# Kernel optimization log

Measured on AMD Instinct MI355X. Metric: run time of the kernel, lower is better.

## Reference

```python
import jax, jax.numpy as jnp
import numpy as np

H = 256           # hidden_size
D_IN = 4 * H      # 1024
D_K = 8 * H       # 2048
B, N = 8, 2048


def setup_inputs() -> dict:
    key = jax.random.key(0)
    ks = jax.random.split(key, 7)
    s_in = 1.0 / np.sqrt(D_IN)
    s_dk = 1.0 / np.sqrt(D_K)
    x = jax.random.normal(ks[0], (B, N, D_IN), dtype=jnp.float32)
    Wq = jax.random.uniform(ks[1], (D_IN, D_K), jnp.float32, -s_in, s_in)
    Wk = jax.random.uniform(ks[2], (D_IN, D_K), jnp.float32, -s_in, s_in)
    Wv = jax.random.uniform(ks[3], (D_IN, D_K), jnp.float32, -s_in, s_in)
    Wfc = jax.random.uniform(ks[4], (D_K, D_IN), jnp.float32, -s_dk, s_dk)
    bfc = jax.random.uniform(ks[5], (D_IN,), jnp.float32, -s_dk, s_dk)
    gamma = jnp.ones((D_IN,), jnp.float32)
    beta = jnp.zeros((D_IN,), jnp.float32)
    return {"x": x, "Wq": Wq, "Wk": Wk, "Wv": Wv, "Wfc": Wfc,
            "bfc": bfc, "gamma": gamma, "beta": beta}


def layer_norm(y, gamma, beta, eps=1e-5):
    mu = jnp.mean(y, axis=-1, keepdims=True)
    var = jnp.var(y, axis=-1, keepdims=True)
    return (y - mu) * jax.lax.rsqrt(var + eps) * gamma + beta


def reference(x, Wq, Wk, Wv, Wfc, bfc, gamma, beta):
    # Q/K/V projections: [B, N, D_K]
    q = jnp.einsum('bnd,dk->bnk', x, Wq)
    k = jnp.einsum('bnd,dk->bnk', x, Wk)
    v = jnp.einsum('bnd,dk->bnk', x, Wv)
    # NOTE: original module has NO 1/sqrt(d_k) scaling — keep it faithful.
    scores = jnp.einsum('bnk,bmk->bnm', q, k)           # [B, N, N]
    attn = jax.nn.softmax(scores, axis=-1)
    att_x = jnp.einsum('bnm,bmk->bnk', attn, v)          # [B, N, D_K]
    h = jax.nn.relu(jnp.einsum('bnk,kd->bnd', att_x, Wfc) + bfc)
    return layer_norm(x + h, gamma, beta)
```

## Files before the change

kernel.cpp:

```cpp
#include <hip/hip_runtime.h>
#include <stdint.h>


#define DEVI __device__ __forceinline__

typedef uint16_t u16;
typedef _Float16 f16x8 __attribute__((ext_vector_type(8)));
typedef float f32x4 __attribute__((ext_vector_type(4)));

DEVI u16 f2h(float f) {
  union { _Float16 h; u16 u; } v;
  v.h = (_Float16)f;
  return v.u;
}
DEVI float h2f(u16 x) {
  union { _Float16 h; u16 u; } v;
  v.u = x;
  return (float)v.h;
}

DEVI void gload_lds16(const void* g, void* lds) {
  __builtin_amdgcn_global_load_lds(
      (const __attribute__((address_space(1))) void*)g,
      (__attribute__((address_space(3))) void*)lds, 16, 0, 0);
}

template <int EPI>
__global__ __launch_bounds__(512, 2) void gemm8p(
    const u16* __restrict__ A, const u16* __restrict__ B, void* __restrict__ C,
    int K, int lda, int ldb, int ldc,
    long aZ, long bZ, long cZ,
    const float* __restrict__ bias, const float* __restrict__ xres)
{
  __shared__ u16 lds[2 * 32768];
  char* ldsB = (char*)lds;
  const int tid = threadIdx.x;
  const int bz = blockIdx.z;

  const int gx = gridDim.x;
  int fl = blockIdx.y * gx + blockIdx.x;
  const int cpx = (gx * gridDim.y) >> 3;
  fl = (fl & 7) * cpx + (fl >> 3);
  const int bx = fl % gx, by = fl / gx;

  const u16* Ab = A + (long)bz * aZ + (long)(by * 256) * lda;
  const u16* Bb = B + (long)bz * bZ + (long)(bx * 256) * ldb;

  const int wid = tid >> 6, lane = tid & 63;
  const int wm = wid >> 2, wn = wid & 3;
  const int l15 = lane & 15;

  int aBase[2][2]; long aoff[2][2];
  int bBase[2][2]; long boff[2][2];
#pragma unroll
  for (int h = 0; h < 2; ++h) {
#pragma unroll
    for (int j = 0; j < 2; ++j) {
      const int s = wid * 2 + j;
      int rs = (s < 8) ? (64 * h + s * 8) : (128 + 64 * h + (s - 8) * 8);
      aBase[h][j] = rs * 128;
      {
        const int d = rs * 128 + lane * 16;
        const int dl = d ^ (((d >> 7) & 7) << 4);
        aoff[h][j] = (long)(dl >> 7) * (lda * 2) + (dl & 127);
      }
      rs = 64 * (s >> 2) + 32 * h + (s & 3) * 8;
      bBase[h][j] = 32768 + rs * 128;
      {
        const int d = rs * 128 + lane * 16;
        const int dl = d ^ (((d >> 7) & 7) << 4);
        boff[h][j] = (long)(dl >> 7) * (ldb * 2) + (dl & 127);
      }
    }
  }

  const int swz = (lane & 7) << 4;
  const int ko0 = ((lane >> 4) * 16) ^ swz;
  const int ko1 = (64 + (lane >> 4) * 16) ^ swz;

  f32x4 acc[8][4] = {};

  auto STAGE_A = [&](int t, int h) {
    char* dst = ldsB + (t & 1) * 65536;
    const long kB = (long)t * 128;
#pragma unroll
    for (int j = 0; j < 2; ++j)
      gload_lds16((const char*)Ab + aoff[h][j] + kB, dst + aBase[h][j]);
  };
  auto STAGE_B = [&](int t, int h) {
    char* dst = ldsB + (t & 1) * 65536;
    const long kB = (long)t * 128;
#pragma unroll
    for (int j = 0; j < 2; ++j)
      gload_lds16((const char*)Bb + boff[h][j] + kB, dst + bBase[h][j]);
  };

  const int NT = K >> 6;
  STAGE_A(0, 0); STAGE_B(0, 0); STAGE_B(0, 1); STAGE_A(0, 1);

  for (int t = 0; t < NT; ++t) {
    const bool more = (t + 1 < NT);
    const char* ab = ldsB + (t & 1) * 65536;
    const char* bb = ab + 32768;
    f16x8 af[8], bf0[4], bf1[4];

    asm volatile("s_waitcnt vmcnt(4)" ::: "memory");
    __builtin_amdgcn_s_barrier();
    if (more) STAGE_A(t + 1, 0);
#pragma unroll
    for (int m = 0; m < 4; ++m) {
      const char* r = ab + (wm * 128 + m * 16 + l15) * 128;
      af[2 * m] = *(const f16x8*)(r + ko0);
      af[2 * m + 1] = *(const f16x8*)(r + ko1);
    }
#pragma unroll
    for (int n = 0; n < 2; ++n) {
      const char* r = bb + (wn * 64 + n * 16 + l15) * 128;
      bf0[2 * n] = *(const f16x8*)(r + ko0);
      bf0[2 * n + 1] = *(const f16x8*)(r + ko1);
    }
    __builtin_amdgcn_s_setprio(1);
#pragma unroll
    for (int ks = 0; ks < 2; ++ks)
#pragma unroll
      for (int m = 0; m < 4; ++m)
#pragma unroll
        for (int n = 0; n < 2; ++n)
          acc[m][n] = __builtin_amdgcn_mfma_f32_16x16x32_f16(
              af[2 * m + ks], bf0[2 * n + ks], acc[m][n], 0, 0, 0);
    __builtin_amdgcn_s_setprio(0);

    if (more) asm volatile("s_waitcnt vmcnt(4)" ::: "memory");
    else      asm volatile("s_waitcnt vmcnt(2)" ::: "memory");
    __builtin_amdgcn_s_barrier();
    if (more) STAGE_B(t + 1, 0);
#pragma unroll
    for (int n = 0; n < 2; ++n) {
      const char* r = bb + (wn * 64 + (n + 2) * 16 + l15) * 128;
      bf1[2 * n] = *(const f16x8*)(r + ko0);
      bf1[2 * n + 1] = *(const f16x8*)(r + ko1);
    }
    __builtin_amdgcn_s_setprio(1);
#pragma unroll
    for (int ks = 0; ks < 2; ++ks)
#pragma unroll
      for (int m = 0; m < 4; ++m)
#pragma unroll
        for (int n = 0; n < 2; ++n)
          acc[m][n + 2] = __builtin_amdgcn_mfma_f32_16x16x32_f16(
              af[2 * m + ks], bf1[2 * n + ks], acc[m][n + 2], 0, 0, 0);
    __builtin_amdgcn_s_setprio(0);

    if (more) asm volatile("s_waitcnt vmcnt(4)" ::: "memory");
    else      asm volatile("s_waitcnt vmcnt(0)" ::: "memory");
    __builtin_amdgcn_s_barrier();
    if (more) STAGE_B(t + 1, 1);
#pragma unroll
    for (int m = 0; m < 4; ++m) {
      const char* r = ab + (wm * 128 + (m + 4) * 16 + l15) * 128;
      af[2 * m] = *(const f16x8*)(r + ko0);
      af[2 * m + 1] = *(const f16x8*)(r + ko1);
    }
    __builtin_amdgcn_s_setprio(1);
#pragma unroll
    for (int ks = 0; ks < 2; ++ks)
#pragma unroll
      for (int m = 0; m < 4; ++m)
#pragma unroll
        for (int n = 0; n < 2; ++n)
          acc[m + 4][n] = __builtin_amdgcn_mfma_f32_16x16x32_f16(
              af[2 * m + ks], bf0[2 * n + ks], acc[m + 4][n], 0, 0, 0);
    __builtin_amdgcn_s_setprio(0);
    if (more) STAGE_A(t + 1, 1);
    __builtin_amdgcn_s_setprio(1);
#pragma unroll
    for (int ks = 0; ks < 2; ++ks)
#pragma unroll
      for (int m = 0; m < 4; ++m)
#pragma unroll
        for (int n = 0; n < 2; ++n)
          acc[m + 4][n + 2] = __builtin_amdgcn_mfma_f32_16x16x32_f16(
              af[2 * m + ks], bf1[2 * n + ks], acc[m + 4][n + 2], 0, 0, 0);
    __builtin_amdgcn_s_setprio(0);
  }

  const long cBase = (long)bz * cZ;
  const int rowBase = by * 256 + wm * 128;
  const int colBase = bx * 256 + wn * 64;

  if constexpr (EPI == 3) {
    u16* vT = (u16*)C;
#pragma unroll
    for (int m = 0; m < 8; ++m) {
      const long row0 = rowBase + m * 16 + (lane >> 4) * 4;
      const long bb2 = (row0 >> 11) * 4194304L + (row0 & 2047);
#pragma unroll
      for (int n = 0; n < 4; ++n) {
        const int col = colBase + n * 16 + l15;
        ushort4 h;
        h.x = f2h(acc[m][n][0]); h.y = f2h(acc[m][n][1]);
        h.z = f2h(acc[m][n][2]); h.w = f2h(acc[m][n][3]);
        *(ushort4*)(vT + bb2 + (long)col * 2048) = h;
      }
    }
  } else {
#pragma unroll
    for (int m = 0; m < 8; ++m) {
#pragma unroll
      for (int r = 0; r < 4; ++r) {
        const long row = rowBase + m * 16 + (lane >> 4) * 4 + r;
#pragma unroll
        for (int n = 0; n < 4; ++n) {
          const int col = colBase + n * 16 + l15;
          float v = acc[m][n][r];
          if constexpr (EPI == 0) {
            ((u16*)C)[cBase + row * ldc + col] = f2h(v);
          } else {
            v += bias[col];
            v = fmaxf(v, 0.0f);
            v += xres[row * (long)ldc + col];
            ((float*)C)[row * (long)ldc + col] = v;
          }
        }
      }
    }
  }
}

template <int EPI>
__global__ __launch_bounds__(256) void gemm_bt(
    const u16* __restrict__ A, const u16* __restrict__ B, void* __restrict__ C,
    int K, int lda, int ldb, int ldc,
    long aZ, long bZ, long cZ,
    const float* __restrict__ bias, const float* __restrict__ xres)
{
  __shared__ u16 sA[128 * 32];
  __shared__ u16 sB[128 * 32];
  const int tid = threadIdx.x;
  const int bz = blockIdx.z;
  const u16* Ab = A + (long)bz * aZ + (long)(blockIdx.y * 128) * lda;
  const u16* Bb = B + (long)bz * bZ + (long)(blockIdx.x * 128) * ldb;

  const int lane = tid & 63;
  const int wr = (tid >> 7) & 1;
  const int wc = (tid >> 6) & 1;
  const int l15 = lane & 15, l4 = lane >> 4;

  const int f0 = tid, f1 = tid + 256;
  const long ga0 = (long)(f0 >> 2) * lda + (f0 & 3) * 8;
  const long ga1 = (long)(f1 >> 2) * lda + (f1 & 3) * 8;
  const long gb0 = (long)(f0 >> 2) * ldb + (f0 & 3) * 8;
  const long gb1 = (long)(f1 >> 2) * ldb + (f1 & 3) * 8;
  u16* sAd0 = sA + (tid & ~63) * 8;
  u16* sAd1 = sA + 2048 + (tid & ~63) * 8;
  u16* sBd0 = sB + (tid & ~63) * 8;
  u16* sBd1 = sB + 2048 + (tid & ~63) * 8;

  f32x4 acc[4][4] = {};

  for (int k0 = 0; k0 < K; k0 += 32) {
    gload_lds16(Ab + ga0 + k0, sAd0);
    gload_lds16(Ab + ga1 + k0, sAd1);
    gload_lds16(Bb + gb0 + k0, sBd0);
    gload_lds16(Bb + gb1 + k0, sBd1);
    __syncthreads();
    f16x8 af[4], bf[4];
#pragma unroll
    for (int m = 0; m < 4; ++m)
      af[m] = *(const f16x8*)(sA + (wr * 64 + m * 16 + l15) * 32 + l4 * 8);
#pragma unroll
    for (int n = 0; n < 4; ++n)
      bf[n] = *(const f16x8*)(sB + (wc * 64 + n * 16 + l15) * 32 + l4 * 8);
#pragma unroll
    for (int m = 0; m < 4; ++m)
#pragma unroll
      for (int n = 0; n < 4; ++n)
        acc[m][n] = __builtin_amdgcn_mfma_f32_16x16x32_f16(af[m], bf[n], acc[m][n], 0, 0, 0);
    __syncthreads();
  }

  const long cBase = (long)bz * cZ;
  const int rowBase = blockIdx.y * 128 + wr * 64;
  const int colBase = blockIdx.x * 128 + wc * 64;

#pragma unroll
  for (int m = 0; m < 4; ++m) {
#pragma unroll
    for (int r = 0; r < 4; ++r) {
      const long row = rowBase + m * 16 + l4 * 4 + r;
#pragma unroll
      for (int n = 0; n < 4; ++n) {
        const int col = colBase + n * 16 + l15;
        float v = acc[m][n][r];
        if constexpr (EPI == 0) {
          ((u16*)C)[cBase + row * ldc + col] = f2h(v);
        } else if constexpr (EPI == 1) {
          ((float*)C)[cBase + row * ldc + col] = v;
        } else {
          v += bias[col];
          v = fmaxf(v, 0.0f);
          v += xres[row * (long)ldc + col];
          ((float*)C)[row * (long)ldc + col] = v;
        }
      }
    }
  }
}

__global__ __launch_bounds__(256) void softmax_rows16(u16* __restrict__ sc)
{
  const long row = blockIdx.x;
  u16* p = sc + row * 2048;
  const int tid = threadIdx.x;
  uint4 w = ((const uint4*)p)[tid];
  float e[8];
  e[0] = h2f(w.x & 0xffff); e[1] = h2f(w.x >> 16);
  e[2] = h2f(w.y & 0xffff); e[3] = h2f(w.y >> 16);
  e[4] = h2f(w.z & 0xffff); e[5] = h2f(w.z >> 16);
  e[6] = h2f(w.w & 0xffff); e[7] = h2f(w.w >> 16);
  float m = fmaxf(fmaxf(fmaxf(e[0], e[1]), fmaxf(e[2], e[3])),
                  fmaxf(fmaxf(e[4], e[5]), fmaxf(e[6], e[7])));
#pragma unroll
  for (int o = 32; o; o >>= 1) m = fmaxf(m, __shfl_xor(m, o));
  __shared__ float redm[4];
  if ((tid & 63) == 0) redm[tid >> 6] = m;
  __syncthreads();
  m = fmaxf(fmaxf(redm[0], redm[1]), fmaxf(redm[2], redm[3]));

  float s = 0.0f;
#pragma unroll
  for (int i = 0; i < 8; ++i) { e[i] = __expf(e[i] - m); s += e[i]; }
#pragma unroll
  for (int o = 32; o; o >>= 1) s += __shfl_xor(s, o);
  __shared__ float reds[4];
  if ((tid & 63) == 0) reds[tid >> 6] = s;
  __syncthreads();
  s = (reds[0] + reds[1]) + (reds[2] + reds[3]);
  const float inv = 1.0f / s;

  uint4 o;
  o.x = (uint32_t)f2h(e[0] * inv) | ((uint32_t)f2h(e[1] * inv) << 16);
  o.y = (uint32_t)f2h(e[2] * inv) | ((uint32_t)f2h(e[3] * inv) << 16);
  o.z = (uint32_t)f2h(e[4] * inv) | ((uint32_t)f2h(e[5] * inv) << 16);
  o.w = (uint32_t)f2h(e[6] * inv) | ((uint32_t)f2h(e[7] * inv) << 16);
  ((uint4*)p)[tid] = o;
}

__global__ __launch_bounds__(256) void softmax_rows(float* __restrict__ scores)
{
  const long row = blockIdx.x;
  const float* src = scores + row * 2048;
  const int tid = threadIdx.x;
  float4 a = ((const float4*)src)[tid];
  float4 b = ((const float4*)src)[tid + 256];
  float m = fmaxf(fmaxf(fmaxf(a.x, a.y), fmaxf(a.z, a.w)),
                  fmaxf(fmaxf(b.x, b.y), fmaxf(b.z, b.w)));
#pragma unroll
  for (int o = 32; o; o >>= 1) m = fmaxf(m, __shfl_xor(m, o));
  __shared__ float redm[4];
  if ((tid & 63) == 0) redm[tid >> 6] = m;
  __syncthreads();
  m = fmaxf(fmaxf(redm[0], redm[1]), fmaxf(redm[2], redm[3]));

  float e[8];
  e[0] = __expf(a.x - m); e[1] = __expf(a.y - m);
  e[2] = __expf(a.z - m); e[3] = __expf(a.w - m);
  e[4] = __expf(b.x - m); e[5] = __expf(b.y - m);
  e[6] = __expf(b.z - m); e[7] = __expf(b.w - m);
  float s = ((e[0] + e[1]) + (e[2] + e[3])) + ((e[4] + e[5]) + (e[6] + e[7]));
#pragma unroll
  for (int o = 32; o; o >>= 1) s += __shfl_xor(s, o);
  __shared__ float reds[4];
  if ((tid & 63) == 0) reds[tid >> 6] = s;
  __syncthreads();
  s = (reds[0] + reds[1]) + (reds[2] + reds[3]);
  const float inv = 1.0f / s;

  u16* dst = (u16*)scores + row * 4096;
  uint2 w0, w1;
  w0.x = (uint32_t)f2h(e[0] * inv) | ((uint32_t)f2h(e[1] * inv) << 16);
  w0.y = (uint32_t)f2h(e[2] * inv) | ((uint32_t)f2h(e[3] * inv) << 16);
  w1.x = (uint32_t)f2h(e[4] * inv) | ((uint32_t)f2h(e[5] * inv) << 16);
  w1.y = (uint32_t)f2h(e[6] * inv) | ((uint32_t)f2h(e[7] * inv) << 16);
  ((uint2*)dst)[tid] = w0;
  ((uint2*)dst)[tid + 256] = w1;
}

__global__ __launch_bounds__(256) void layernorm_rows(
    const float* __restrict__ y, const float* __restrict__ gamma,
    const float* __restrict__ beta, float* __restrict__ out)
{
  const long row = blockIdx.x;
  const int tid = threadIdx.x;
  float4 v = ((const float4*)(y + row * 1024))[tid];
  float s = (v.x + v.y) + (v.z + v.w);
  float q = (v.x * v.x + v.y * v.y) + (v.z * v.z + v.w * v.w);
#pragma unroll
  for (int o = 32; o; o >>= 1) { s += __shfl_xor(s, o); q += __shfl_xor(q, o); }
  __shared__ float rs[4], rq[4];
  if ((tid & 63) == 0) { rs[tid >> 6] = s; rq[tid >> 6] = q; }
  __syncthreads();
  s = (rs[0] + rs[1]) + (rs[2] + rs[3]);
  q = (rq[0] + rq[1]) + (rq[2] + rq[3]);
  const float mu = s * (1.0f / 1024.0f);
  const float var = q * (1.0f / 1024.0f) - mu * mu;
  const float rstd = rsqrtf(var + 1e-5f);
  float4 g = ((const float4*)gamma)[tid];
  float4 be = ((const float4*)beta)[tid];
  float4 o;
  o.x = (v.x - mu) * rstd * g.x + be.x;
  o.y = (v.y - mu) * rstd * g.y + be.y;
  o.z = (v.z - mu) * rstd * g.z + be.z;
  o.w = (v.w - mu) * rstd * g.w + be.w;
  __syncthreads();
  ((float4*)(out + row * 1024))[tid] = o;
}

__global__ __launch_bounds__(256) void cvt_f32_f16(
    const float* __restrict__ in, u16* __restrict__ out, long n4)
{
  const long stride = (long)gridDim.x * 256;
  for (long i = (long)blockIdx.x * 256 + threadIdx.x; i < n4; i += stride) {
    float4 v = ((const float4*)in)[i];
    uint2 p;
    p.x = (uint32_t)f2h(v.x) | ((uint32_t)f2h(v.y) << 16);
    p.y = (uint32_t)f2h(v.z) | ((uint32_t)f2h(v.w) << 16);
    ((uint2*)out)[i] = p;
  }
}

__global__ __launch_bounds__(256) void tw_f32(
    const float* __restrict__ in, u16* __restrict__ out, int R, int C)
{
  __shared__ float T[32][33];
  const int c0 = blockIdx.x * 32, r0 = blockIdx.y * 32;
  const int tx = threadIdx.x & 31, ty = threadIdx.x >> 5;
#pragma unroll
  for (int i = 0; i < 4; ++i)
    T[ty + i * 8][tx] = in[(long)(r0 + ty + i * 8) * C + c0 + tx];
  __syncthreads();
#pragma unroll
  for (int i = 0; i < 4; ++i)
    out[(long)(c0 + ty + i * 8) * R + r0 + tx] = f2h(T[tx][ty + i * 8]);
}

__global__ __launch_bounds__(256) void transpose_u16(
    const u16* __restrict__ in, u16* __restrict__ out, int R, int C)
{
  __shared__ u16 T[32][33];
  const long zo = (long)blockIdx.z * R * C;
  const int c0 = blockIdx.x * 32, r0 = blockIdx.y * 32;
  const int tx = threadIdx.x & 31, ty = threadIdx.x >> 5;
#pragma unroll
  for (int i = 0; i < 4; ++i)
    T[ty + i * 8][tx] = in[zo + (long)(r0 + ty + i * 8) * C + c0 + tx];
  __syncthreads();
#pragma unroll
  for (int i = 0; i < 4; ++i)
    out[zo + (long)(c0 + ty + i * 8) * R + r0 + tx] = T[tx][ty + i * 8];
}

extern "C" void kernel_launch(void* const* d_in, const int* in_sizes, int n_in,
                              void* d_out, int out_size, void* d_ws, size_t ws_size,
                              hipStream_t stream)
{
  const float* x     = (const float*)d_in[0];
  const float* Wq    = (const float*)d_in[1];
  const float* Wk    = (const float*)d_in[2];
  const float* Wv    = (const float*)d_in[3];
  const float* Wfc   = (const float*)d_in[4];
  const float* bfc   = (const float*)d_in[5];
  const float* gamma = (const float*)d_in[6];
  const float* beta  = (const float*)d_in[7];
  float* out = (float*)d_out;

  char* ws = (char*)d_ws;

  u16* wqkvT = (u16*)(ws + 0);
  u16* wfcT  = (u16*)(ws + 12582912);
  tw_f32<<<dim3(64, 32), 256, 0, stream>>>(Wq, wqkvT, 1024, 2048);
  tw_f32<<<dim3(64, 32), 256, 0, stream>>>(Wk, wqkvT + (long)2048 * 1024, 1024, 2048);
  tw_f32<<<dim3(64, 32), 256, 0, stream>>>(Wv, wqkvT + (long)2 * 2048 * 1024, 1024, 2048);
  tw_f32<<<dim3(32, 64), 256, 0, stream>>>(Wfc, wfcT, 2048, 1024);

  if (ws_size >= 251658240ULL) {
    u16*  q_   = (u16*)(ws + 16777216);
    u16*  k_   = (u16*)(ws + 83886080);
    u16*  vT   = (u16*)(ws + 150994944);
    u16*  sc16 = (u16*)(ws + 218103808);
    u16*  xb   = sc16;

    cvt_f32_f16<<<2048, 256, 0, stream>>>(x, xb, (long)16384 * 1024 / 4);

    gemm8p<0><<<dim3(8, 64, 2), 512, 0, stream>>>(
        xb, wqkvT, (void*)q_, 1024, 1024, 1024, 2048,
        0L, (long)2048 * 1024, (long)16384 * 2048, nullptr, nullptr);
    gemm8p<3><<<dim3(8, 64, 1), 512, 0, stream>>>(
        xb, wqkvT + (long)2 * 2048 * 1024, (void*)vT, 1024, 1024, 1024, 2048,
        0L, 0L, 0L, nullptr, nullptr);

    for (int c = 0; c < 2; ++c) {
      const u16* qc = q_ + (long)c * 1024 * 2048;
      gemm8p<0><<<dim3(8, 4, 8), 512, 0, stream>>>(
          qc, k_, (void*)sc16, 2048, 2048, 2048, 2048,
          (long)2048 * 2048, (long)2048 * 2048, (long)1024 * 2048, nullptr, nullptr);
      softmax_rows16<<<8192, 256, 0, stream>>>(sc16);
      gemm8p<0><<<dim3(8, 4, 8), 512, 0, stream>>>(
          sc16, vT, (void*)(q_ + (long)c * 1024 * 2048), 2048, 2048, 2048, 2048,
          (long)1024 * 2048, (long)2048 * 2048, (long)2048 * 2048, nullptr, nullptr);
    }

    gemm8p<2><<<dim3(4, 64, 1), 512, 0, stream>>>(
        q_, wfcT, (void*)out, 2048, 2048, 2048, 1024,
        0L, 0L, 0L, bfc, x);
  } else if (ws_size >= 109051904ULL) {
    u16*  xb2 = (u16*)(ws + 16777216);
    u16*  q2  = (u16*)(ws + 25165824);
    u16*  k2  = q2 + (long)2 * 2048 * 2048;
    u16*  v2  = q2 + (long)4 * 2048 * 2048;
    float* sc2 = (float*)(ws + 75497472);
    u16*  vT2   = k2;
    u16*  attx2 = q2;

    for (int p = 0; p < 4; ++p) {
      const float* xp = x + (long)p * 4096 * 1024;
      cvt_f32_f16<<<1024, 256, 0, stream>>>(xp, xb2, (long)4096 * 1024 / 4);
      for (int b = 0; b < 2; ++b)
        gemm_bt<0><<<dim3(16, 16, 3), 256, 0, stream>>>(
            xb2 + (long)b * 2048 * 1024, wqkvT, (void*)(q2 + (long)b * 2048 * 2048),
            1024, 1024, 1024, 2048,
            0L, (long)2048 * 1024, (long)2 * 2048 * 2048, nullptr, nullptr);
      gemm_bt<1><<<dim3(16, 16, 2), 256, 0, stream>>>(
          q2, k2, (void*)sc2, 2048, 2048, 2048, 2048,
          (long)2048 * 2048, (long)2048 * 2048, (long)2048 * 2048, nullptr, nullptr);
      softmax_rows<<<4096, 256, 0, stream>>>(sc2);
      transpose_u16<<<dim3(64, 64, 2), 256, 0, stream>>>(v2, vT2, 2048, 2048);
      gemm_bt<0><<<dim3(16, 16, 2), 256, 0, stream>>>(
          (const u16*)sc2, vT2, (void*)attx2, 2048, 4096, 2048, 2048,
          (long)2048 * 4096, (long)2048 * 2048, (long)2048 * 2048, nullptr, nullptr);
      gemm_bt<2><<<dim3(8, 32, 1), 256, 0, stream>>>(
          attx2, wfcT, (void*)(out + (long)p * 4096 * 1024), 2048, 2048, 2048, 1024,
          0L, 0L, 0L, bfc, xp);
    }
  } else {
    u16*  xb_b   = (u16*)(ws + 16777216);
    u16*  qkv_b  = (u16*)(ws + 20971520);
    u16*  q_b    = qkv_b;
    u16*  k_b    = qkv_b + (long)2048 * 2048;
    u16*  v_b    = qkv_b + (long)2 * 2048 * 2048;
    float* sc_b  = (float*)(ws + 46137344);
    u16*  vT_b   = k_b;
    u16*  attx_b = q_b;

    for (int b = 0; b < 8; ++b) {
      const float* x_b = x + (long)b * 2048 * 1024;
      cvt_f32_f16<<<512, 256, 0, stream>>>(x_b, xb_b, (long)2048 * 1024 / 4);
      gemm_bt<0><<<dim3(16, 16, 3), 256, 0, stream>>>(
          xb_b, wqkvT, (void*)qkv_b, 1024, 1024, 1024, 2048,
          0L, (long)2048 * 1024, (long)2048 * 2048, nullptr, nullptr);
      gemm_bt<1><<<dim3(16, 16, 1), 256, 0, stream>>>(
          q_b, k_b, (void*)sc_b, 2048, 2048, 2048, 2048,
          0L, 0L, 0L, nullptr, nullptr);
      softmax_rows<<<2048, 256, 0, stream>>>(sc_b);
      transpose_u16<<<dim3(64, 64, 1), 256, 0, stream>>>(v_b, vT_b, 2048, 2048);
      gemm_bt<0><<<dim3(16, 16, 1), 256, 0, stream>>>(
          (const u16*)sc_b, vT_b, (void*)attx_b, 2048, 4096, 2048, 2048,
          0L, 0L, 0L, nullptr, nullptr);
      gemm_bt<2><<<dim3(8, 16, 1), 256, 0, stream>>>(
          attx_b, wfcT, (void*)(out + (long)b * 2048 * 1024), 2048, 2048, 2048, 1024,
          0L, 0L, 0L, bfc, x_b);
    }
  }

  layernorm_rows<<<16384, 256, 0, stream>>>(out, gamma, beta, out);
}
```

Baseline: 626.8 us.

## Prefetch next tile's first fragments and deepen global-to-LDS staging in GEMM loop

```diff
diff --git a/kernel.cpp b/kernel.cpp
--- a/kernel.cpp
+++ b/kernel.cpp
@@ -96,22 +96,21 @@
   };
 
   const int NT = K >> 6;
+
+  f16x8 afA[8], afB[8], bf0[4], bf1[4];
+
   STAGE_A(0, 0); STAGE_B(0, 0); STAGE_B(0, 1); STAGE_A(0, 1);
-
-  for (int t = 0; t < NT; ++t) {
-    const bool more = (t + 1 < NT);
-    const char* ab = ldsB + (t & 1) * 65536;
+  STAGE_A(1, 0); STAGE_B(1, 0);
+  asm volatile("s_waitcnt vmcnt(8)" ::: "memory");
+  __builtin_amdgcn_s_barrier();
+  {
+    const char* ab = ldsB;
     const char* bb = ab + 32768;
-    f16x8 af[8], bf0[4], bf1[4];
-
-    asm volatile("s_waitcnt vmcnt(4)" ::: "memory");
-    __builtin_amdgcn_s_barrier();
-    if (more) STAGE_A(t + 1, 0);
 #pragma unroll
     for (int m = 0; m < 4; ++m) {
       const char* r = ab + (wm * 128 + m * 16 + l15) * 128;
-      af[2 * m] = *(const f16x8*)(r + ko0);
-      af[2 * m + 1] = *(const f16x8*)(r + ko1);
+      afA[2 * m] = *(const f16x8*)(r + ko0);
+      afA[2 * m + 1] = *(const f16x8*)(r + ko1);
     }
 #pragma unroll
     for (int n = 0; n < 2; ++n) {
@@ -119,21 +118,19 @@
       bf0[2 * n] = *(const f16x8*)(r + ko0);
       bf0[2 * n + 1] = *(const f16x8*)(r + ko1);
     }
-    __builtin_amdgcn_s_setprio(1);
-#pragma unroll
-    for (int ks = 0; ks < 2; ++ks)
-#pragma unroll
-      for (int m = 0; m < 4; ++m)
-#pragma unroll
-        for (int n = 0; n < 2; ++n)
-          acc[m][n] = __builtin_amdgcn_mfma_f32_16x16x32_f16(
-              af[2 * m + ks], bf0[2 * n + ks], acc[m][n], 0, 0, 0);
-    __builtin_amdgcn_s_setprio(0);
-
-    if (more) asm volatile("s_waitcnt vmcnt(4)" ::: "memory");
+  }
+
+  for (int t = 0; t < NT; ++t) {
+    const bool more = (t + 1 < NT);
+    const bool more2 = (t + 2 < NT);
+    const char* ab = ldsB + (t & 1) * 65536;
+    const char* bb = ab + 32768;
+    const char* abN = ldsB + ((t + 1) & 1) * 65536;
+    const char* bbN = abN + 32768;
+
+    if (more) asm volatile("s_waitcnt vmcnt(6)" ::: "memory");
     else      asm volatile("s_waitcnt vmcnt(2)" ::: "memory");
     __builtin_amdgcn_s_barrier();
-    if (more) STAGE_B(t + 1, 0);
 #pragma unroll
     for (int n = 0; n < 2; ++n) {
       const char* r = bb + (wn * 64 + (n + 2) * 16 + l15) * 128;
@@ -147,20 +144,32 @@
       for (int m = 0; m < 4; ++m)
 #pragma unroll
         for (int n = 0; n < 2; ++n)
-          acc[m][n + 2] = __builtin_amdgcn_mfma_f32_16x16x32_f16(
-              af[2 * m + ks], bf1[2 * n + ks], acc[m][n + 2], 0, 0, 0);
+          acc[m][n] = __builtin_amdgcn_mfma_f32_16x16x32_f16(
+              afA[2 * m + ks], bf0[2 * n + ks], acc[m][n], 0, 0, 0);
     __builtin_amdgcn_s_setprio(0);
 
     if (more) asm volatile("s_waitcnt vmcnt(4)" ::: "memory");
     else      asm volatile("s_waitcnt vmcnt(0)" ::: "memory");
     __builtin_amdgcn_s_barrier();
-    if (more) STAGE_B(t + 1, 1);
 #pragma unroll
     for (int m = 0; m < 4; ++m) {
       const char* r = ab + (wm * 128 + (m + 4) * 16 + l15) * 128;
-      af[2 * m] = *(const f16x8*)(r + ko0);
-      af[2 * m + 1] = *(const f16x8*)(r + ko1);
-    }
+      afB[2 * m] = *(const f16x8*)(r + ko0);
+      afB[2 * m + 1] = *(const f16x8*)(r + ko1);
+    }
+    if (more) STAGE_B(t + 1, 1);
+    __builtin_amdgcn_s_setprio(1);
+#pragma unroll
+    for (int ks = 0; ks < 2; ++ks)
+#pragma unroll
+      for (int m = 0; m < 4; ++m)
+#pragma unroll
+        for (int n = 0; n < 2; ++n)
+          acc[m][n + 2] = __builtin_amdgcn_mfma_f32_16x16x32_f16(
+              afA[2 * m + ks], bf1[2 * n + ks], acc[m][n + 2], 0, 0, 0);
+    __builtin_amdgcn_s_setprio(0);
+
+    if (more) STAGE_A(t + 1, 1);
     __builtin_amdgcn_s_setprio(1);
 #pragma unroll
     for (int ks = 0; ks < 2; ++ks)
@@ -169,9 +178,26 @@
 #pragma unroll
         for (int n = 0; n < 2; ++n)
           acc[m + 4][n] = __builtin_amdgcn_mfma_f32_16x16x32_f16(
-              af[2 * m + ks], bf0[2 * n + ks], acc[m + 4][n], 0, 0, 0);
+              afB[2 * m + ks], bf0[2 * n + ks], acc[m + 4][n], 0, 0, 0);
     __builtin_amdgcn_s_setprio(0);
-    if (more) STAGE_A(t + 1, 1);
+
+    if (more) {
+      asm volatile("s_waitcnt vmcnt(4)" ::: "memory");
+      __builtin_amdgcn_s_barrier();
+#pragma unroll
+      for (int m = 0; m < 4; ++m) {
+        const char* r = abN + (wm * 128 + m * 16 + l15) * 128;
+        afA[2 * m] = *(const f16x8*)(r + ko0);
+        afA[2 * m + 1] = *(const f16x8*)(r + ko1);
+      }
+#pragma unroll
+      for (int n = 0; n < 2; ++n) {
+        const char* r = bbN + (wn * 64 + n * 16 + l15) * 128;
+        bf0[2 * n] = *(const f16x8*)(r + ko0);
+        bf0[2 * n + 1] = *(const f16x8*)(r + ko1);
+      }
+      if (more2) { STAGE_A(t + 2, 0); STAGE_B(t + 2, 0); }
+    }
     __builtin_amdgcn_s_setprio(1);
 #pragma unroll
     for (int ks = 0; ks < 2; ++ks)
@@ -180,7 +206,7 @@
 #pragma unroll
         for (int n = 0; n < 2; ++n)
           acc[m + 4][n + 2] = __builtin_amdgcn_mfma_f32_16x16x32_f16(
-              af[2 * m + ks], bf1[2 * n + ks], acc[m + 4][n + 2], 0, 0, 0);
+              afB[2 * m + ks], bf1[2 * n + ks], acc[m + 4][n + 2], 0, 0, 0);
     __builtin_amdgcn_s_setprio(0);
   }
 
```

Result: slower. 650.9 us (+3.8%).

## Deepen GEMM prefetch pipeline to two K-tiles in flight with unrolled loop

Applied to the files above, without the earlier changes.

```diff
diff --git a/kernel.cpp b/kernel.cpp
--- a/kernel.cpp
+++ b/kernel.cpp
@@ -25,8 +25,13 @@
       (__attribute__((address_space(3))) void*)lds, 16, 0, 0);
 }
 
+#define GATE_S(N) do { asm volatile("s_waitcnt vmcnt(" #N ")" ::: "memory"); \
+                       __builtin_amdgcn_s_barrier(); } while (0)
+#define LGKM0 do { asm volatile("s_waitcnt lgkmcnt(0)" ::: "memory"); \
+                   __builtin_amdgcn_sched_barrier(0); } while (0)
+
 template <int EPI>
-__global__ __launch_bounds__(512, 2) void gemm8p(
+__global__ __launch_bounds__(512, 2) void gemm8x(
     const u16* __restrict__ A, const u16* __restrict__ B, void* __restrict__ C,
     int K, int lda, int ldb, int ldc,
     long aZ, long bZ, long cZ,
@@ -94,31 +99,40 @@
     for (int j = 0; j < 2; ++j)
       gload_lds16((const char*)Bb + boff[h][j] + kB, dst + bBase[h][j]);
   };
+  auto RD_A = [&](const char* base, int mh, f16x8* dst) {
+#pragma unroll
+    for (int m = 0; m < 4; ++m) {
+      const char* r = base + (wm * 128 + (mh * 4 + m) * 16 + l15) * 128;
+      dst[2 * m] = *(const f16x8*)(r + ko0);
+      dst[2 * m + 1] = *(const f16x8*)(r + ko1);
+    }
+  };
+  auto RD_B = [&](const char* base, int nh, f16x8* dst) {
+#pragma unroll
+    for (int n = 0; n < 2; ++n) {
+      const char* r = base + 32768 + (wn * 64 + (nh * 2 + n) * 16 + l15) * 128;
+      dst[2 * n] = *(const f16x8*)(r + ko0);
+      dst[2 * n + 1] = *(const f16x8*)(r + ko1);
+    }
+  };
 
   const int NT = K >> 6;
+  const int NI = NT >> 1;
+
   STAGE_A(0, 0); STAGE_B(0, 0); STAGE_B(0, 1); STAGE_A(0, 1);
-
-  for (int t = 0; t < NT; ++t) {
-    const bool more = (t + 1 < NT);
-    const char* ab = ldsB + (t & 1) * 65536;
-    const char* bb = ab + 32768;
-    f16x8 af[8], bf0[4], bf1[4];
-
-    asm volatile("s_waitcnt vmcnt(4)" ::: "memory");
-    __builtin_amdgcn_s_barrier();
-    if (more) STAGE_A(t + 1, 0);
-#pragma unroll
-    for (int m = 0; m < 4; ++m) {
-      const char* r = ab + (wm * 128 + m * 16 + l15) * 128;
-      af[2 * m] = *(const f16x8*)(r + ko0);
-      af[2 * m + 1] = *(const f16x8*)(r + ko1);
-    }
-#pragma unroll
-    for (int n = 0; n < 2; ++n) {
-      const char* r = bb + (wn * 64 + n * 16 + l15) * 128;
-      bf0[2 * n] = *(const f16x8*)(r + ko0);
-      bf0[2 * n + 1] = *(const f16x8*)(r + ko1);
-    }
+  STAGE_A(1, 0); STAGE_B(1, 0); STAGE_B(1, 1);
+
+  for (int i = 0; i < NI; ++i) {
+    const bool last = (i + 1 == NI);
+    const int ta = 2 * i, tb = 2 * i + 1;
+    const char* buf0 = ldsB;
+    const char* buf1 = ldsB + 65536;
+    f16x8 af[8], b0v[4], b1v[4];
+
+    GATE_S(10);
+    RD_A(buf0, 0, af); RD_B(buf0, 0, b0v);
+    STAGE_A(tb, 1);
+    LGKM0;
     __builtin_amdgcn_s_setprio(1);
 #pragma unroll
     for (int ks = 0; ks < 2; ++ks)
@@ -127,19 +141,14 @@
 #pragma unroll
         for (int n = 0; n < 2; ++n)
           acc[m][n] = __builtin_amdgcn_mfma_f32_16x16x32_f16(
-              af[2 * m + ks], bf0[2 * n + ks], acc[m][n], 0, 0, 0);
-    __builtin_amdgcn_s_setprio(0);
-
-    if (more) asm volatile("s_waitcnt vmcnt(4)" ::: "memory");
-    else      asm volatile("s_waitcnt vmcnt(2)" ::: "memory");
-    __builtin_amdgcn_s_barrier();
-    if (more) STAGE_B(t + 1, 0);
-#pragma unroll
-    for (int n = 0; n < 2; ++n) {
-      const char* r = bb + (wn * 64 + (n + 2) * 16 + l15) * 128;
-      bf1[2 * n] = *(const f16x8*)(r + ko0);
-      bf1[2 * n + 1] = *(const f16x8*)(r + ko1);
-    }
+              af[2 * m + ks], b0v[2 * n + ks], acc[m][n], 0, 0, 0);
+    __builtin_amdgcn_s_setprio(0);
+    __builtin_amdgcn_s_barrier();
+
+    GATE_S(10);
+    RD_B(buf0, 1, b1v);
+    if (!last) STAGE_A(ta + 2, 0);
+    LGKM0;
     __builtin_amdgcn_s_setprio(1);
 #pragma unroll
     for (int ks = 0; ks < 2; ++ks)
@@ -148,19 +157,14 @@
 #pragma unroll
         for (int n = 0; n < 2; ++n)
           acc[m][n + 2] = __builtin_amdgcn_mfma_f32_16x16x32_f16(
-              af[2 * m + ks], bf1[2 * n + ks], acc[m][n + 2], 0, 0, 0);
-    __builtin_amdgcn_s_setprio(0);
-
-    if (more) asm volatile("s_waitcnt vmcnt(4)" ::: "memory");
-    else      asm volatile("s_waitcnt vmcnt(0)" ::: "memory");
-    __builtin_amdgcn_s_barrier();
-    if (more) STAGE_B(t + 1, 1);
-#pragma unroll
-    for (int m = 0; m < 4; ++m) {
-      const char* r = ab + (wm * 128 + (m + 4) * 16 + l15) * 128;
-      af[2 * m] = *(const f16x8*)(r + ko0);
-      af[2 * m + 1] = *(const f16x8*)(r + ko1);
-    }
+              af[2 * m + ks], b1v[2 * n + ks], acc[m][n + 2], 0, 0, 0);
+    __builtin_amdgcn_s_setprio(0);
+    __builtin_amdgcn_s_barrier();
+
+    if (!last) GATE_S(10); else GATE_S(8);
+    RD_A(buf0, 1, af);
+    if (!last) STAGE_B(ta + 2, 0);
+    LGKM0;
     __builtin_amdgcn_s_setprio(1);
 #pragma unroll
     for (int ks = 0; ks < 2; ++ks)
@@ -169,9 +173,11 @@
 #pragma unroll
         for (int n = 0; n < 2; ++n)
           acc[m + 4][n] = __builtin_amdgcn_mfma_f32_16x16x32_f16(
-              af[2 * m + ks], bf0[2 * n + ks], acc[m + 4][n], 0, 0, 0);
-    __builtin_amdgcn_s_setprio(0);
-    if (more) STAGE_A(t + 1, 1);
+              af[2 * m + ks], b0v[2 * n + ks], acc[m + 4][n], 0, 0, 0);
+    __builtin_amdgcn_s_setprio(0);
+    __builtin_amdgcn_s_barrier();
+
+    if (!last) STAGE_B(ta + 2, 1);
     __builtin_amdgcn_s_setprio(1);
 #pragma unroll
     for (int ks = 0; ks < 2; ++ks)
@@ -180,8 +186,70 @@
 #pragma unroll
         for (int n = 0; n < 2; ++n)
           acc[m + 4][n + 2] = __builtin_amdgcn_mfma_f32_16x16x32_f16(
-              af[2 * m + ks], bf1[2 * n + ks], acc[m + 4][n + 2], 0, 0, 0);
-    __builtin_amdgcn_s_setprio(0);
+              af[2 * m + ks], b1v[2 * n + ks], acc[m + 4][n + 2], 0, 0, 0);
+    __builtin_amdgcn_s_setprio(0);
+    __builtin_amdgcn_s_barrier();
+
+    if (!last) GATE_S(10); else GATE_S(4);
+    RD_A(buf1, 0, af); RD_B(buf1, 0, b0v);
+    if (!last) STAGE_A(ta + 2, 1);
+    LGKM0;
+    __builtin_amdgcn_s_setprio(1);
+#pragma unroll
+    for (int ks = 0; ks < 2; ++ks)
+#pragma unroll
+      for (int m = 0; m < 4; ++m)
+#pragma unroll
+        for (int n = 0; n < 2; ++n)
+          acc[m][n] = __builtin_amdgcn_mfma_f32_16x16x32_f16(
+              af[2 * m + ks], b0v[2 * n + ks], acc[m][n], 0, 0, 0);
+    __builtin_amdgcn_s_setprio(0);
+    __builtin_amdgcn_s_barrier();
+
+    if (!last) GATE_S(10); else GATE_S(2);
+    RD_B(buf1, 1, b1v);
+    if (!last) STAGE_A(tb + 2, 0);
+    LGKM0;
+    __builtin_amdgcn_s_setprio(1);
+#pragma unroll
+    for (int ks = 0; ks < 2; ++ks)
+#pragma unroll
+      for (int m = 0; m < 4; ++m)
+#pragma unroll
+        for (int n = 0; n < 2; ++n)
+          acc[m][n + 2] = __builtin_amdgcn_mfma_f32_16x16x32_f16(
+              af[2 * m + ks], b1v[2 * n + ks], acc[m][n + 2], 0, 0, 0);
+    __builtin_amdgcn_s_setprio(0);
+    __builtin_amdgcn_s_barrier();
+
+    if (!last) GATE_S(10); else GATE_S(0);
+    RD_A(buf1, 1, af);
+    if (!last) STAGE_B(tb + 2, 0);
+    LGKM0;
+    __builtin_amdgcn_s_setprio(1);
+#pragma unroll
+    for (int ks = 0; ks < 2; ++ks)
+#pragma unroll
+      for (int m = 0; m < 4; ++m)
+#pragma unroll
+        for (int n = 0; n < 2; ++n)
+          acc[m + 4][n] = __builtin_amdgcn_mfma_f32_16x16x32_f16(
+              af[2 * m + ks], b0v[2 * n + ks], acc[m + 4][n], 0, 0, 0);
+    __builtin_amdgcn_s_setprio(0);
+    __builtin_amdgcn_s_barrier();
+
+    if (!last) STAGE_B(tb + 2, 1);
+    __builtin_amdgcn_s_setprio(1);
+#pragma unroll
+    for (int ks = 0; ks < 2; ++ks)
+#pragma unroll
+      for (int m = 0; m < 4; ++m)
+#pragma unroll
+        for (int n = 0; n < 2; ++n)
+          acc[m + 4][n + 2] = __builtin_amdgcn_mfma_f32_16x16x32_f16(
+              af[2 * m + ks], b1v[2 * n + ks], acc[m + 4][n + 2], 0, 0, 0);
+    __builtin_amdgcn_s_setprio(0);
+    __builtin_amdgcn_s_barrier();
   }
 
   const long cBase = (long)bz * cZ;
@@ -492,25 +560,25 @@
 
     cvt_f32_f16<<<2048, 256, 0, stream>>>(x, xb, (long)16384 * 1024 / 4);
 
-    gemm8p<0><<<dim3(8, 64, 2), 512, 0, stream>>>(
+    gemm8x<0><<<dim3(8, 64, 2), 512, 0, stream>>>(
         xb, wqkvT, (void*)q_, 1024, 1024, 1024, 2048,
         0L, (long)2048 * 1024, (long)16384 * 2048, nullptr, nullptr);
-    gemm8p<3><<<dim3(8, 64, 1), 512, 0, stream>>>(
+    gemm8x<3><<<dim3(8, 64, 1), 512, 0, stream>>>(
         xb, wqkvT + (long)2 * 2048 * 1024, (void*)vT, 1024, 1024, 1024, 2048,
         0L, 0L, 0L, nullptr, nullptr);
 
     for (int c = 0; c < 2; ++c) {
       const u16* qc = q_ + (long)c * 1024 * 2048;
-      gemm8p<0><<<dim3(8, 4, 8), 512, 0, stream>>>(
+      gemm8x<0><<<dim3(8, 4, 8), 512, 0, stream>>>(
           qc, k_, (void*)sc16, 2048, 2048, 2048, 2048,
           (long)2048 * 2048, (long)2048 * 2048, (long)1024 * 2048, nullptr, nullptr);
       softmax_rows16<<<8192, 256, 0, stream>>>(sc16);
-      gemm8p<0><<<dim3(8, 4, 8), 512, 0, stream>>>(
+      gemm8x<0><<<dim3(8, 4, 8), 512, 0, stream>>>(
           sc16, vT, (void*)(q_ + (long)c * 1024 * 2048), 2048, 2048, 2048, 2048,
           (long)1024 * 2048, (long)2048 * 2048, (long)2048 * 2048, nullptr, nullptr);
     }
 
-    gemm8p<2><<<dim3(4, 64, 1), 512, 0, stream>>>(
+    gemm8x<2><<<dim3(4, 64, 1), 512, 0, stream>>>(
         q_, wfcT, (void*)out, 2048, 2048, 2048, 1024,
         0L, 0L, 0L, bfc, x);
   } else if (ws_size >= 109051904ULL) {
```

New measurement: 600.2 us. 4.2% less time.
